# Kernel optimization log

Hardware: AMD Instinct MI355X
Metric: run time of the kernel (lower is better)

## Reference

```python
import jax, jax.numpy as jnp
import numpy as np

NUM_HEADS = 12

def setup_inputs() -> dict:
    key = jax.random.key(0)
    ks = jax.random.split(key, 6)
    B, N, C = 16, 1024, 768
    H, d = NUM_HEADS, C // NUM_HEADS
    return {
        "x": jax.random.normal(ks[0], (B, N, C), dtype=jnp.float32),
        "W_qkv": jax.random.normal(ks[1], (C, 3 * C), dtype=jnp.float32) * 0.02,
        "b_qkv": jax.random.normal(ks[2], (3 * C,), dtype=jnp.float32) * 0.02,
        "zeta": jnp.ones((1, 1, H, 1, d), dtype=jnp.float32),
        "W_proj": jax.random.normal(ks[3], (C, C), dtype=jnp.float32) * 0.02,
        "b_proj": jax.random.normal(ks[4], (C,), dtype=jnp.float32) * 0.02,
        "mask": jnp.zeros((B, N), dtype=bool),
    }

def reference(x, W_qkv, b_qkv, zeta, W_proj, b_proj, mask):
    B, N, C = x.shape
    H = NUM_HEADS
    d = C // H
    scale = d ** -0.5
    # qkv: (B,N,3C) -> (B,N,3,H,d) -> (3,B,H,N,d), gated by zeta (1,1,H,1,d)
    qkv = (x @ W_qkv + b_qkv).reshape(B, N, 3, H, d).transpose(2, 0, 3, 1, 4)
    qkv = qkv * zeta
    q, k, v = qkv[0], qkv[1], qkv[2]
    attn = jnp.einsum("bhnd,bhmd->bhnm", q, k) * scale
    # mask (B,N) over keys -> (B,1,1,N)
    attn = jnp.where(mask[:, None, None, :], -jnp.inf, attn)
    attn = jax.nn.softmax(attn, axis=-1)
    out = jnp.einsum("bhnm,bhmd->bhnd", attn, v)          # (B,H,N,d)
    out = out.transpose(0, 2, 1, 3).reshape(B, N, C)
    return out @ W_proj + b_proj
```

## Files before the change

### kernel.cpp

```cpp
#include <hip/hip_runtime.h>
#include <hip/hip_bf16.h>

typedef unsigned short ushort_t;
typedef __bf16 bf16_t;
typedef bf16_t bf16x8 __attribute__((ext_vector_type(8)));
typedef float floatx4 __attribute__((ext_vector_type(4)));
typedef ushort_t ushortx8 __attribute__((ext_vector_type(8)));

struct alignas(8) us4 { ushort_t x, y, z, w; };

__device__ __forceinline__ ushort_t f2bf(float f) {
  union { float f; unsigned int u; } v; v.f = f;
  unsigned int u = v.u;
  return (ushort_t)((u + 0x7fffu + ((u >> 16) & 1u)) >> 16);
}

__device__ __forceinline__ unsigned int pk_bf16(float a, float b) {
  __hip_bfloat162 h = __float22bfloat162_rn(float2{a, b});
  union { __hip_bfloat162 h; unsigned int u; } v; v.h = h;
  return v.u;
}

__device__ __forceinline__ void async16(const void* g, void* l) {
  __builtin_amdgcn_global_load_lds(
      (const __attribute__((address_space(1))) unsigned int*)g,
      (__attribute__((address_space(3))) unsigned int*)l, 16, 0, 0);
}

#define LOG2E 1.44269504088896340736f


__global__ __launch_bounds__(256) void k_prep(const float* __restrict__ x,
                                              ushort_t* __restrict__ xb,
                                              const float* __restrict__ Wq,
                                              ushort_t* __restrict__ WqT,
                                              const float* __restrict__ Wp,
                                              ushort_t* __restrict__ WpT) {
  __shared__ float tile[32][33];
  const int bid = blockIdx.x, t = threadIdx.x;
  if (bid < 6144) {
    size_t i = ((size_t)bid * 256 + t) * 8;
    float4 a = *(const float4*)(x + i);
    float4 b = *(const float4*)(x + i + 4);
    ushortx8 o;
    o[0] = f2bf(a.x); o[1] = f2bf(a.y); o[2] = f2bf(a.z); o[3] = f2bf(a.w);
    o[4] = f2bf(b.x); o[5] = f2bf(b.y); o[6] = f2bf(b.z); o[7] = f2bf(b.w);
    *(ushortx8*)(xb + i) = o;
    return;
  }
  const float* in; ushort_t* out; int C, c0, r0;
  if (bid < 7872) {
    int b2 = bid - 6144;
    in = Wq; out = WqT; C = 2304;
    c0 = (b2 % 72) * 32; r0 = (b2 / 72) * 32;
  } else {
    int b3 = bid - 7872;
    in = Wp; out = WpT; C = 768;
    c0 = (b3 % 24) * 32; r0 = (b3 / 24) * 32;
  }
  const int tx = t & 31, ty = t >> 5;
#pragma unroll
  for (int i = 0; i < 32; i += 8)
    tile[ty + i][tx] = in[(size_t)(r0 + ty + i) * C + c0 + tx];
  __syncthreads();
#pragma unroll
  for (int i = 0; i < 32; i += 8)
    out[(size_t)(c0 + ty + i) * 768 + r0 + tx] = f2bf(tile[tx][ty + i]);
}


template <bool SWAP>
__device__ __forceinline__ void gemm_pipe2(const ushort_t* __restrict__ A,
                                           const ushort_t* __restrict__ Bt,
                                           int m0, int n0,
                                           ushort_t* sA, ushort_t* sB,
                                           floatx4 acc[8][4]) {
  const int t = threadIdx.x;
  const int lane = t & 63;
  const int lr = lane & 15, qd = lane >> 4;
  const int w = t >> 6;
  const int wr = w >> 1, wc = w & 1;
  const int swz = ((t & 3) ^ ((t >> 3) & 3)) * 8;
  const ushort_t* gA = A + (size_t)(m0 + (t >> 2)) * 768 + swz;
  const ushort_t* gB = Bt + (size_t)(n0 + (t >> 2)) * 768 + swz;
  char* lA = (char*)sA + t * 16;
  char* lB = (char*)sB + t * 16;
  const int rsz = (qd ^ ((lr >> 1) & 3)) * 16;
#define ISSUE(kk, buf)                                    \
  do {                                                    \
    const int k0_ = (kk) * 32;                            \
    const int ba_ = (buf) * 16384, bb_ = (buf) * 8192;    \
    async16(gA + k0_, lA + ba_);                          \
    async16(gA + k0_ + 64 * 768, lA + ba_ + 4096);        \
    async16(gA + k0_ + 128 * 768, lA + ba_ + 8192);       \
    async16(gA + k0_ + 192 * 768, lA + ba_ + 12288);      \
    async16(gB + k0_, lB + bb_);                          \
    async16(gB + k0_ + 64 * 768, lB + bb_ + 4096);        \
  } while (0)
  ISSUE(0, 0);
  asm volatile("s_waitcnt vmcnt(0)" ::: "memory");
  asm volatile("s_barrier" ::: "memory");
#pragma unroll
  for (int k = 0; k < 24; ++k) {
    if (k + 1 < 24) ISSUE(k + 1, (k + 1) & 1);
    const char* cA = (const char*)sA + (k & 1) * 16384;
    const char* cB = (const char*)sB + (k & 1) * 8192;
    bf16x8 af[8], bfr[4];
#pragma unroll
    for (int i = 0; i < 8; ++i)
      af[i] = *(const bf16x8*)(cA + (wr * 128 + i * 16 + lr) * 64 + rsz);
#pragma unroll
    for (int j = 0; j < 4; ++j)
      bfr[j] = *(const bf16x8*)(cB + (wc * 64 + j * 16 + lr) * 64 + rsz);
#pragma unroll
    for (int i = 0; i < 8; ++i)
#pragma unroll
      for (int j = 0; j < 4; ++j) {
        if constexpr (SWAP)
          acc[i][j] = __builtin_amdgcn_mfma_f32_16x16x32_bf16(bfr[j], af[i], acc[i][j], 0, 0, 0);
        else
          acc[i][j] = __builtin_amdgcn_mfma_f32_16x16x32_bf16(af[i], bfr[j], acc[i][j], 0, 0, 0);
      }
    if (k + 1 < 24)
      asm volatile("s_waitcnt vmcnt(0)" ::: "memory");
    if (k < 23) asm volatile("s_barrier" ::: "memory");
  }
#undef ISSUE
}


__global__ __launch_bounds__(256, 2) void k_qkv(const ushort_t* __restrict__ xb,
                                                const ushort_t* __restrict__ WqT,
                                                const float* __restrict__ bqkv,
                                                const float* __restrict__ zeta,
                                                ushort_t* __restrict__ qb,
                                                ushort_t* __restrict__ kb,
                                                ushort_t* __restrict__ vtb) {
  __shared__ alignas(16) ushort_t sA[2 * 8192];
  __shared__ alignas(16) ushort_t sB[2 * 4096];
  floatx4 acc[8][4] = {};
  const int lin = blockIdx.x;
  const int xcd = lin & 7, idx = lin >> 3;
  const int m0 = (xcd * 8 + (idx & 7)) * 256;
  const int n0 = (idx >> 3) * 128;
  const int tq = n0 / 768;
  const int t = threadIdx.x, lane = t & 63, w = t >> 6;
  const int wr = w >> 1, wc = w & 1, lr = lane & 15, qd = lane >> 4;
  if (tq < 2) {
    gemm_pipe2<true>(xb, WqT, m0, n0, sA, sB, acc);
    ushort_t* dst = (tq == 0) ? qb : kb;
    const float sc = (tq == 0) ? 0.125f * LOG2E : 1.0f;
#pragma unroll
    for (int j = 0; j < 4; ++j) {
      int n = n0 + wc * 64 + j * 16 + qd * 4;
      int nc = n - tq * 768;
      int h = nc >> 6, dim = n & 63;
      float4 b4 = *(const float4*)&bqkv[n];
      float4 z4 = *(const float4*)&zeta[nc];
      float g0 = z4.x * sc, g1 = z4.y * sc, g2 = z4.z * sc, g3 = z4.w * sc;
#pragma unroll
      for (int i = 0; i < 8; ++i) {
        int m = m0 + wr * 128 + i * 16 + lr;
        int b = m >> 10, seq = m & 1023;
        us4 pk;
        pk.x = f2bf((acc[i][j][0] + b4.x) * g0);
        pk.y = f2bf((acc[i][j][1] + b4.y) * g1);
        pk.z = f2bf((acc[i][j][2] + b4.z) * g2);
        pk.w = f2bf((acc[i][j][3] + b4.w) * g3);
        *(us4*)&dst[(((size_t)b * 12 + h) * 1024 + seq) * 64 + dim] = pk;
      }
    }
  } else {
    gemm_pipe2<false>(xb, WqT, m0, n0, sA, sB, acc);
#pragma unroll
    for (int j = 0; j < 4; ++j) {
      int n = n0 + wc * 64 + j * 16 + lr;
      int nc = n - 2 * 768;
      int h = nc >> 6, dim = n & 63;
      float bias = bqkv[n];
      float zv = zeta[nc];
#pragma unroll
      for (int i = 0; i < 8; ++i) {
        int mbase = m0 + wr * 128 + i * 16 + qd * 4;
        int b = mbase >> 10, seq = mbase & 1023;
        us4 pk;
        pk.x = f2bf((acc[i][j][0] + bias) * zv);
        pk.y = f2bf((acc[i][j][1] + bias) * zv);
        pk.z = f2bf((acc[i][j][2] + bias) * zv);
        pk.w = f2bf((acc[i][j][3] + bias) * zv);
        *(us4*)&vtb[(((size_t)b * 12 + h) * 64 + dim) * 1024 + seq] = pk;
      }
    }
  }
}


__global__ __launch_bounds__(256, 3) void k_attn(const ushort_t* __restrict__ qg,
                                                 const ushort_t* __restrict__ kg,
                                                 const ushort_t* __restrict__ vg,
                                                 const unsigned char* __restrict__ mask,
                                                 ushort_t* __restrict__ ob) {
  __shared__ alignas(16) char smem[49664];
  char* sV = smem + 32768;
  float* maskadd = (float*)(smem + 49152);
  const int t = threadIdx.x, lane = t & 63, w = t >> 6;
  const int lr = lane & 15, qd = lane >> 4;
  const int lin = blockIdx.x;
  const int bh = (lin & 7) + 8 * (lin >> 6);
  const int qt = (lin >> 3) & 7;
  const int b = bh / 12, h = bh % 12;
  const int qrow0 = qt * 128 + w * 32;
  const ushort_t* qp = qg + (size_t)bh * 65536;
  const ushort_t* kp = kg + (size_t)bh * 65536;
  const ushort_t* vp = vg + (size_t)bh * 65536;
  const unsigned char* mp = mask + b * 1024;

  bf16x8 qf[2][2];
#pragma unroll
  for (int ns = 0; ns < 2; ++ns)
#pragma unroll
    for (int kk = 0; kk < 2; ++kk)
      qf[ns][kk] = *(const bf16x8*)(qp + (size_t)(qrow0 + ns * 16 + lr) * 64 + kk * 32 + qd * 8);

  floatx4 o[4][2] = {};
  float lst[2] = {0.f, 0.f};
  char* sPw = smem + 16384 + w * 4096;

  for (int kt = 0; kt < 8; ++kt) {
    __syncthreads();
    const ushort_t* kpt = kp + kt * 8192;
#pragma unroll
    for (int it = 0; it < 4; ++it) {
      int p = it * 256 + t;
      int r = p >> 3, cs = (p & 7) ^ (r & 7);
      async16(kpt + r * 64 + cs * 8, smem + p * 16);
    }
    const ushort_t* vpt = vp + kt * 128;
#pragma unroll
    for (int it = 0; it < 4; ++it) {
      int p = it * 256 + t;
      int r = p >> 4, cs = (p & 15) ^ (r & 15);
      async16(vpt + (size_t)r * 1024 + cs * 8, sV + p * 16);
    }
    if (t < 128) maskadd[t] = mp[kt * 128 + t] ? -1e30f : 0.0f;
    asm volatile("s_waitcnt vmcnt(0)" ::: "memory");
    __syncthreads();

#pragma unroll
    for (int hh = 0; hh < 2; ++hh) {
      floatx4 s[4][2] = {};
#pragma unroll
      for (int kk = 0; kk < 2; ++kk) {
#pragma unroll
        for (int ms = 0; ms < 4; ++ms) {
          bf16x8 ak = *(const bf16x8*)(smem + ((hh * 4 + ms) * 16 + lr) * 128 +
                                       ((kk * 4 + qd) ^ (lr & 7)) * 16);
#pragma unroll
          for (int ns = 0; ns < 2; ++ns)
            s[ms][ns] = __builtin_amdgcn_mfma_f32_16x16x32_bf16(ak, qf[ns][kk], s[ms][ns], 0, 0, 0);
        }
      }
#pragma unroll
      for (int ms = 0; ms < 4; ++ms) {
        float4 mk = *(const float4*)&maskadd[(hh * 4 + ms) * 16 + qd * 4];
#pragma unroll
        for (int ns = 0; ns < 2; ++ns) {
          float p0 = __builtin_amdgcn_exp2f(s[ms][ns][0] + mk.x);
          float p1 = __builtin_amdgcn_exp2f(s[ms][ns][1] + mk.y);
          float p2 = __builtin_amdgcn_exp2f(s[ms][ns][2] + mk.z);
          float p3 = __builtin_amdgcn_exp2f(s[ms][ns][3] + mk.w);
          lst[ns] += (p0 + p1) + (p2 + p3);
          uint2 pk;
          pk.x = pk_bf16(p0, p1);
          pk.y = pk_bf16(p2, p3);
          *(uint2*)(sPw + (ns * 16 + lr) * 128 +
                    ((ms * 2 + (qd >> 1)) ^ (lr & 7)) * 16 + (qd & 1) * 8) = pk;
        }
      }
      asm volatile("s_waitcnt lgkmcnt(0)" ::: "memory");
#pragma unroll
      for (int kk = 0; kk < 2; ++kk) {
        bf16x8 pb[2];
#pragma unroll
        for (int ns = 0; ns < 2; ++ns)
          pb[ns] = *(const bf16x8*)(sPw + (ns * 16 + lr) * 128 +
                                    ((kk * 4 + qd) ^ (lr & 7)) * 16);
#pragma unroll
        for (int ds = 0; ds < 4; ++ds) {
          bf16x8 av = *(const bf16x8*)(sV + (ds * 16 + lr) * 256 +
                                       ((hh * 8 + kk * 4 + qd) ^ lr) * 16);
#pragma unroll
          for (int ns = 0; ns < 2; ++ns)
            o[ds][ns] = __builtin_amdgcn_mfma_f32_16x16x32_bf16(av, pb[ns], o[ds][ns], 0, 0, 0);
        }
      }
    }
  }
#pragma unroll
  for (int ns = 0; ns < 2; ++ns) {
    lst[ns] += __shfl_xor(lst[ns], 16);
    lst[ns] += __shfl_xor(lst[ns], 32);
  }
#pragma unroll
  for (int ns = 0; ns < 2; ++ns) {
    float rl = 1.0f / lst[ns];
    size_t row = (size_t)(b * 1024 + qrow0 + ns * 16 + lr) * 768 + h * 64;
#pragma unroll
    for (int ds = 0; ds < 4; ++ds) {
      uint2 ov;
      ov.x = pk_bf16(o[ds][ns][0] * rl, o[ds][ns][1] * rl);
      ov.y = pk_bf16(o[ds][ns][2] * rl, o[ds][ns][3] * rl);
      *(uint2*)&ob[row + ds * 16 + qd * 4] = ov;
    }
  }
}


__global__ __launch_bounds__(256, 2) void k_proj(const ushort_t* __restrict__ ob,
                                                 const ushort_t* __restrict__ WpT,
                                                 const float* __restrict__ bproj,
                                                 float* __restrict__ out) {
  __shared__ alignas(16) ushort_t sA[2 * 8192];
  __shared__ alignas(16) ushort_t sB[2 * 4096];
  floatx4 acc[8][4] = {};
  const int lin = blockIdx.x;
  const int xcd = lin & 7, idx = lin >> 3;
  const int m0 = (xcd * 8 + (idx & 7)) * 256;
  const int n0 = (idx >> 3) * 128;
  gemm_pipe2<true>(ob, WpT, m0, n0, sA, sB, acc);
  const int t = threadIdx.x, lane = t & 63, w = t >> 6;
  const int wr = w >> 1, wc = w & 1, lr = lane & 15, qd = lane >> 4;
#pragma unroll
  for (int j = 0; j < 4; ++j) {
    int n = n0 + wc * 64 + j * 16 + qd * 4;
    float4 b4 = *(const float4*)&bproj[n];
#pragma unroll
    for (int i = 0; i < 8; ++i) {
      int m = m0 + wr * 128 + i * 16 + lr;
      float4 o;
      o.x = acc[i][j][0] + b4.x;
      o.y = acc[i][j][1] + b4.y;
      o.z = acc[i][j][2] + b4.z;
      o.w = acc[i][j][3] + b4.w;
      *(float4*)&out[(size_t)m * 768 + n] = o;
    }
  }
}


extern "C" void kernel_launch(void* const* d_in, const int* in_sizes, int n_in,
                              void* d_out, int out_size, void* d_ws, size_t ws_size,
                              hipStream_t stream) {
  const float* x = (const float*)d_in[0];
  const float* bqkv = (const float*)d_in[2];
  const float* zeta = (const float*)d_in[3];
  const float* bproj = (const float*)d_in[5];
  const unsigned char* mask = (const unsigned char*)d_in[6];
  float* out = (float*)d_out;
  char* ws = (char*)d_ws;
  ushort_t* xb  = (ushort_t*)(ws);
  ushort_t* WqT = (ushort_t*)(ws + 25165824);
  ushort_t* WpT = (ushort_t*)(ws + 28704768);
  ushort_t* qb  = (ushort_t*)(ws + 29884416);
  ushort_t* kb  = (ushort_t*)(ws + 55050240);
  ushort_t* vtb = (ushort_t*)(ws + 80216064);
  ushort_t* ob  = xb;

  k_prep<<<dim3(8448), dim3(256), 0, stream>>>(x, xb, (const float*)d_in[1], WqT,
                                               (const float*)d_in[4], WpT);
  k_qkv<<<dim3(1152), dim3(256), 0, stream>>>(xb, WqT, bqkv, zeta, qb, kb, vtb);
  k_attn<<<dim3(1536), dim3(256), 0, stream>>>(qb, kb, vtb, mask, ob);
  k_proj<<<dim3(384), dim3(256), 0, stream>>>(ob, WpT, bproj, out);
}
```

Baseline: 303.1 us.

## Double-buffer K/V tiles in attention kernel and raise GEMM occupancy bounds

The attention kernel now walks the keys in 16 tiles of 64 instead of 8 tiles of 128. The K and V tiles are double-buffered in LDS, so the next tile's async loads overlap compute on the current tile. The mask is converted once up front instead of on every tile. MFMA sections are wrapped in setprio hints, and there is one barrier per tile in place of two. The QKV and projection GEMMs get launch_bounds raised from 2 to 3 blocks per SM, which risks register spills in exchange for more occupancy.

```diff
diff --git a/kernel.cpp b/kernel.cpp
--- a/kernel.cpp
+++ b/kernel.cpp
@@ -129,7 +129,7 @@
 }
 
 
-__global__ __launch_bounds__(256, 2) void k_qkv(const ushort_t* __restrict__ xb,
+__global__ __launch_bounds__(256, 3) void k_qkv(const ushort_t* __restrict__ xb,
                                                 const ushort_t* __restrict__ WqT,
                                                 const float* __restrict__ bqkv,
                                                 const float* __restrict__ zeta,
@@ -200,8 +200,7 @@
                                                  const ushort_t* __restrict__ vg,
                                                  const unsigned char* __restrict__ mask,
                                                  ushort_t* __restrict__ ob) {
-  __shared__ alignas(16) char smem[49664];
-  char* sV = smem + 32768;
+  __shared__ alignas(16) char smem[53248];
   float* maskadd = (float*)(smem + 49152);
   const int t = threadIdx.x, lane = t & 63, w = t >> 6;
   const int lr = lane & 15, qd = lane >> 4;
@@ -224,78 +223,103 @@
 
   floatx4 o[4][2] = {};
   float lst[2] = {0.f, 0.f};
-  char* sPw = smem + 16384 + w * 4096;
-
-  for (int kt = 0; kt < 8; ++kt) {
-    __syncthreads();
-    const ushort_t* kpt = kp + kt * 8192;
-#pragma unroll
-    for (int it = 0; it < 4; ++it) {
-      int p = it * 256 + t;
-      int r = p >> 3, cs = (p & 7) ^ (r & 7);
-      async16(kpt + r * 64 + cs * 8, smem + p * 16);
-    }
-    const ushort_t* vpt = vp + kt * 128;
-#pragma unroll
-    for (int it = 0; it < 4; ++it) {
-      int p = it * 256 + t;
-      int r = p >> 4, cs = (p & 15) ^ (r & 15);
-      async16(vpt + (size_t)r * 1024 + cs * 8, sV + p * 16);
-    }
-    if (t < 128) maskadd[t] = mp[kt * 128 + t] ? -1e30f : 0.0f;
-    asm volatile("s_waitcnt vmcnt(0)" ::: "memory");
-    __syncthreads();
-
-#pragma unroll
-    for (int hh = 0; hh < 2; ++hh) {
-      floatx4 s[4][2] = {};
-#pragma unroll
-      for (int kk = 0; kk < 2; ++kk) {
-#pragma unroll
-        for (int ms = 0; ms < 4; ++ms) {
-          bf16x8 ak = *(const bf16x8*)(smem + ((hh * 4 + ms) * 16 + lr) * 128 +
-                                       ((kk * 4 + qd) ^ (lr & 7)) * 16);
-#pragma unroll
-          for (int ns = 0; ns < 2; ++ns)
-            s[ms][ns] = __builtin_amdgcn_mfma_f32_16x16x32_bf16(ak, qf[ns][kk], s[ms][ns], 0, 0, 0);
-        }
-      }
+  char* sPw = smem + 32768 + w * 4096;
+
+  {
+    uchar4 mv = *(const uchar4*)(mp + t * 4);
+    float4 f;
+    f.x = mv.x ? -1e30f : 0.0f;
+    f.y = mv.y ? -1e30f : 0.0f;
+    f.z = mv.z ? -1e30f : 0.0f;
+    f.w = mv.w ? -1e30f : 0.0f;
+    *(float4*)&maskadd[t * 4] = f;
+  }
+
+#define STAGE(kt_, st_)                                                   \
+  do {                                                                    \
+    const ushort_t* kpt_ = kp + (kt_) * 4096;                             \
+    const ushort_t* vpt_ = vp + (kt_) * 64;                               \
+    _Pragma("unroll")                                                     \
+    for (int it = 0; it < 2; ++it) {                                      \
+      int p = it * 256 + t;                                               \
+      int r = p >> 3, cs = (p & 7) ^ (r & 7);                             \
+      async16(kpt_ + r * 64 + cs * 8, smem + (st_) * 16384 + p * 16);     \
+      async16(vpt_ + (size_t)r * 1024 + cs * 8,                           \
+              smem + (st_) * 16384 + 8192 + p * 16);                      \
+    }                                                                     \
+  } while (0)
+
+  STAGE(0, 0);
+  __syncthreads();
+
+#pragma unroll 2
+  for (int kt = 0; kt < 16; ++kt) {
+    const int st = kt & 1;
+    if (kt + 1 < 16) STAGE(kt + 1, st ^ 1);
+    const char* sK = smem + st * 16384;
+    const char* sV = smem + st * 16384 + 8192;
+
+    floatx4 s[4][2] = {};
+    __builtin_amdgcn_s_setprio(1);
+#pragma unroll
+    for (int kk = 0; kk < 2; ++kk) {
 #pragma unroll
       for (int ms = 0; ms < 4; ++ms) {
-        float4 mk = *(const float4*)&maskadd[(hh * 4 + ms) * 16 + qd * 4];
-#pragma unroll
-        for (int ns = 0; ns < 2; ++ns) {
-          float p0 = __builtin_amdgcn_exp2f(s[ms][ns][0] + mk.x);
-          float p1 = __builtin_amdgcn_exp2f(s[ms][ns][1] + mk.y);
-          float p2 = __builtin_amdgcn_exp2f(s[ms][ns][2] + mk.z);
-          float p3 = __builtin_amdgcn_exp2f(s[ms][ns][3] + mk.w);
-          lst[ns] += (p0 + p1) + (p2 + p3);
-          uint2 pk;
-          pk.x = pk_bf16(p0, p1);
-          pk.y = pk_bf16(p2, p3);
-          *(uint2*)(sPw + (ns * 16 + lr) * 128 +
-                    ((ms * 2 + (qd >> 1)) ^ (lr & 7)) * 16 + (qd & 1) * 8) = pk;
-        }
-      }
-      asm volatile("s_waitcnt lgkmcnt(0)" ::: "memory");
-#pragma unroll
-      for (int kk = 0; kk < 2; ++kk) {
-        bf16x8 pb[2];
+        bf16x8 ak = *(const bf16x8*)(sK + (ms * 16 + lr) * 128 +
+                                     ((kk * 4 + qd) ^ (lr & 7)) * 16);
 #pragma unroll
         for (int ns = 0; ns < 2; ++ns)
-          pb[ns] = *(const bf16x8*)(sPw + (ns * 16 + lr) * 128 +
-                                    ((kk * 4 + qd) ^ (lr & 7)) * 16);
-#pragma unroll
-        for (int ds = 0; ds < 4; ++ds) {
-          bf16x8 av = *(const bf16x8*)(sV + (ds * 16 + lr) * 256 +
-                                       ((hh * 8 + kk * 4 + qd) ^ lr) * 16);
-#pragma unroll
-          for (int ns = 0; ns < 2; ++ns)
-            o[ds][ns] = __builtin_amdgcn_mfma_f32_16x16x32_bf16(av, pb[ns], o[ds][ns], 0, 0, 0);
-        }
-      }
-    }
-  }
+          s[ms][ns] = __builtin_amdgcn_mfma_f32_16x16x32_bf16(ak, qf[ns][kk], s[ms][ns], 0, 0, 0);
+      }
+    }
+    __builtin_amdgcn_s_setprio(0);
+
+#pragma unroll
+    for (int ms = 0; ms < 4; ++ms) {
+      float4 mk = *(const float4*)&maskadd[kt * 64 + ms * 16 + qd * 4];
+#pragma unroll
+      for (int ns = 0; ns < 2; ++ns) {
+        float p0 = __builtin_amdgcn_exp2f(s[ms][ns][0] + mk.x);
+        float p1 = __builtin_amdgcn_exp2f(s[ms][ns][1] + mk.y);
+        float p2 = __builtin_amdgcn_exp2f(s[ms][ns][2] + mk.z);
+        float p3 = __builtin_amdgcn_exp2f(s[ms][ns][3] + mk.w);
+        lst[ns] += (p0 + p1) + (p2 + p3);
+        uint2 pk;
+        pk.x = pk_bf16(p0, p1);
+        pk.y = pk_bf16(p2, p3);
+        *(uint2*)(sPw + (ns * 16 + lr) * 128 +
+                  ((ms * 2 + (qd >> 1)) ^ (lr & 7)) * 16 + (qd & 1) * 8) = pk;
+      }
+    }
+    asm volatile("s_waitcnt lgkmcnt(0)" ::: "memory");
+    __builtin_amdgcn_sched_barrier(0);
+
+    __builtin_amdgcn_s_setprio(1);
+#pragma unroll
+    for (int kk = 0; kk < 2; ++kk) {
+      bf16x8 pb[2];
+#pragma unroll
+      for (int ns = 0; ns < 2; ++ns)
+        pb[ns] = *(const bf16x8*)(sPw + (ns * 16 + lr) * 128 +
+                                  ((kk * 4 + qd) ^ (lr & 7)) * 16);
+#pragma unroll
+      for (int ds = 0; ds < 4; ++ds) {
+        bf16x8 av = *(const bf16x8*)(sV + (ds * 16 + lr) * 128 +
+                                     ((kk * 4 + qd) ^ (lr & 7)) * 16);
+#pragma unroll
+        for (int ns = 0; ns < 2; ++ns)
+          o[ds][ns] = __builtin_amdgcn_mfma_f32_16x16x32_bf16(av, pb[ns], o[ds][ns], 0, 0, 0);
+      }
+    }
+    __builtin_amdgcn_s_setprio(0);
+
+    if (kt + 1 < 16) {
+      asm volatile("s_waitcnt vmcnt(0)" ::: "memory");
+      asm volatile("s_barrier" ::: "memory");
+    }
+  }
+#undef STAGE
+
 #pragma unroll
   for (int ns = 0; ns < 2; ++ns) {
     lst[ns] += __shfl_xor(lst[ns], 16);
@@ -316,7 +340,7 @@
 }
 
 
-__global__ __launch_bounds__(256, 2) void k_proj(const ushort_t* __restrict__ ob,
+__global__ __launch_bounds__(256, 3) void k_proj(const ushort_t* __restrict__ ob,
                                                  const ushort_t* __restrict__ WpT,
                                                  const float* __restrict__ bproj,
                                                  float* __restrict__ out) {
```

After: 482.9 us. 59.3% more time.
